# Optimization experiments

Measured on AMD Instinct MI355X. Metric: run time of the kernel, lower is better.

Reference implementation:

```python
import jax, jax.numpy as jnp
import numpy as np

B, S, D, H = 2, 2048, 1024, 16
HD = D // H          # head dim = 64
BASE = 10000.0
SCALE = 1.0 / np.sqrt(HD)


def setup_inputs() -> dict:
    key = jax.random.key(0)
    ks = jax.random.split(key, 7)
    mk = lambda k, shp: (jax.random.normal(k, shp, dtype=jnp.float32) * 0.02)
    return {
        "hidden_states": jax.random.normal(ks[0], (B, S, D), dtype=jnp.float32),
        "Wq": mk(ks[1], (D, D)), "bq": jnp.zeros((D,), jnp.float32),
        "Wk": mk(ks[2], (D, D)), "bk": jnp.zeros((D,), jnp.float32),
        "Wv": mk(ks[3], (D, D)), "bv": jnp.zeros((D,), jnp.float32),
    }


def _rope_tables(seq_len, head_dim, dtype):
    # Intended RoPE: inv_freq over head_dim/2 frequencies.
    # (Original torch code has an off-by-2 indexing bug that makes it un-runnable
    #  for head_dim > 2; we implement the intended standard RoPE:
    #  inv_freq = base^{-arange(0, head_dim, 2)/head_dim}, length head_dim//2.)
    dim_half = head_dim // 2
    inv_freq = 1.0 / (BASE ** (jnp.arange(dim_half, dtype=dtype) / dim_half))
    ang = jnp.arange(seq_len, dtype=dtype)[:, None] * inv_freq[None, :]  # [S, dim_half]
    return jnp.sin(ang), jnp.cos(ang)


def _apply_rope(x, sin, cos):
    # x: [B, H, S, HD]; sin/cos: [S, HD//2]
    dim_half = x.shape[-1] // 2
    x1, x2 = x[..., :dim_half], x[..., dim_half:]
    sin = sin[None, None]  # [1,1,S,dim_half]
    cos = cos[None, None]
    return jnp.concatenate([x1 * cos - x2 * sin, x1 * sin + x2 * cos], axis=-1)


def reference(hidden_states, Wq, bq, Wk, bk, Wv, bv):
    b, s, d = hidden_states.shape
    # QKV projections (nn.Linear: x @ W.T + b), then split heads -> [B,H,S,HD]
    def proj(W, bias):
        y = jnp.einsum("bsd,ed->bse", hidden_states, W) + bias
        return y.reshape(b, s, H, HD).transpose(0, 2, 1, 3)

    q, k, v = proj(Wq, bq), proj(Wk, bk), proj(Wv, bv)

    sin, cos = _rope_tables(s, HD, hidden_states.dtype)
    q = _apply_rope(q, sin, cos)
    k = _apply_rope(k, sin, cos)

    # Non-causal SDPA, scale = 1/sqrt(head_dim), no mask, eval mode (no dropout)
    scores = jnp.einsum("bhqd,bhkd->bhqk", q, k) * SCALE
    probs = jax.nn.softmax(scores, axis=-1)
    ctx = jnp.einsum("bhqk,bhkd->bhqd", probs, v)

    # [B,H,S,HD] -> [B,S,D]
    return ctx.transpose(0, 2, 1, 3).reshape(b, s, d)
```

## Files before the change

kernel.cpp:

```cpp
#include <hip/hip_runtime.h>
#include <hip/hip_bf16.h>
#include <math.h>

#define B_  2
#define S_  2048
#define D_  1024
#define H_  16
#define HD_ 64
#define M_  (B_*S_)
#define N3  (3*D_)
#define K_  D_
#define LOG2E 1.44269504088896340736f

typedef unsigned short u16;
typedef __bf16 bf16x8 __attribute__((ext_vector_type(8)));
typedef float  f32x4  __attribute__((ext_vector_type(4)));
typedef float  f32x16 __attribute__((ext_vector_type(16)));
typedef unsigned short u16x4 __attribute__((ext_vector_type(4)));
typedef unsigned short u16x8 __attribute__((ext_vector_type(8)));
typedef unsigned int   u32x4v __attribute__((ext_vector_type(4)));

typedef const __attribute__((address_space(1))) unsigned int gu32;
typedef __attribute__((address_space(3)))       unsigned int lu32;

__device__ __forceinline__ void gload_lds16(const void* g, void* l) {
  __builtin_amdgcn_global_load_lds((gu32*)g, (lu32*)l, 16, 0, 0);
}

__device__ __forceinline__ u16 f2bf(float f) {
  unsigned u = __builtin_bit_cast(unsigned, f);
  u += 0x7fffu + ((u >> 16) & 1u);
  return (u16)(u >> 16);
}

__device__ __forceinline__ unsigned pk2(float lo, float hi) {
  unsigned d;
  asm("v_cvt_pk_bf16_f32 %0, %1, %2" : "=v"(d) : "v"(lo), "v"(hi));
  return d;
}

__global__ void k_prep(const float* __restrict__ hs, const float* __restrict__ Wq,
                       const float* __restrict__ Wk, const float* __restrict__ Wv,
                       u16* __restrict__ Xb, u16* __restrict__ Wb) {
  const int NX = M_*D_/4, NW = D_*D_/4;
  int i = blockIdx.x * blockDim.x + threadIdx.x;
  const float4* src; u16* dst; int off;
  if (i < NX)            { src = (const float4*)hs; dst = Xb;           off = i; }
  else if (i < NX+NW)    { src = (const float4*)Wq; dst = Wb;           off = i-NX; }
  else if (i < NX+2*NW)  { src = (const float4*)Wk; dst = Wb + D_*D_;   off = i-NX-NW; }
  else                   { src = (const float4*)Wv; dst = Wb + 2*D_*D_; off = i-NX-2*NW; }
  float4 v = src[off];
  ushort4 o; o.x = f2bf(v.x); o.y = f2bf(v.y); o.z = f2bf(v.z); o.w = f2bf(v.w);
  reinterpret_cast<ushort4*>(dst)[off] = o;
}

__global__ void k_tables(float* __restrict__ sinT, float* __restrict__ cosT) {
  int gid = blockIdx.x * blockDim.x + threadIdx.x;
  int s = gid >> 5, j = gid & 31;
  float invf = (float)exp(-(double)j * (log(10000.0) / 32.0));
  float angf = (float)s * invf;
  double ang = (double)angf;
  sinT[gid] = (float)sin(ang);
  cosT[gid] = (float)cos(ang);
}

#define BM 128
#define BN 128
#define BK 64

__global__ __launch_bounds__(256) void k_gemm(const u16* __restrict__ A,
                                              const u16* __restrict__ Bm,
                                              const float* __restrict__ bq,
                                              const float* __restrict__ bk,
                                              const float* __restrict__ bv,
                                              const float* __restrict__ sinT,
                                              const float* __restrict__ cosT,
                                              u16* __restrict__ Qo,
                                              u16* __restrict__ Ko,
                                              u16* __restrict__ Vo) {
  __shared__ alignas(16) u16 As[BM*BK];
  __shared__ alignas(16) u16 Bs[BN*BK];
  const int t = threadIdx.x;
  const int l = t & 63, w = t >> 6;
  const int wr = w >> 1, wc = w & 1;
  const int lr = l & 15, lg = l >> 4;

  const int lin = blockIdx.y * (N3/BN) + blockIdx.x;
  const int wk  = (lin & 7) * 96 + (lin >> 3);
  const int m0 = (wk / (N3/BN)) * BM, n0 = (wk % (N3/BN)) * BN;

  f32x4 acc[4][4] = {};

  for (int k0 = 0; k0 < K_; k0 += BK) {
#pragma unroll
    for (int i = 0; i < 4; ++i) {
      int chunk = i*256 + t;
      int row = chunk >> 3, kc = chunk & 7;
      gload_lds16(A + (size_t)(m0+row)*K_ + k0 + kc*8, &As[chunk*8]);
    }
#pragma unroll
    for (int i = 0; i < 4; ++i) {
      int chunk = i*256 + t;
      int row = chunk >> 3, kc = chunk & 7;
      gload_lds16(Bm + (size_t)(n0+row)*K_ + k0 + kc*8, &Bs[chunk*8]);
    }
    __syncthreads();
#pragma unroll
    for (int ks = 0; ks < 2; ++ks) {
      bf16x8 a[4], b[4];
#pragma unroll
      for (int m = 0; m < 4; ++m)
        a[m] = *reinterpret_cast<const bf16x8*>(&As[(wr*64 + m*16 + lr)*BK + ks*32 + lg*8]);
#pragma unroll
      for (int n = 0; n < 4; ++n)
        b[n] = *reinterpret_cast<const bf16x8*>(&Bs[(wc*64 + n*16 + lr)*BK + ks*32 + lg*8]);
#pragma unroll
      for (int m = 0; m < 4; ++m)
#pragma unroll
        for (int n = 0; n < 4; ++n)
          acc[m][n] = __builtin_amdgcn_mfma_f32_16x16x32_bf16(a[m], b[n], acc[m][n], 0, 0, 0);
    }
    __syncthreads();
  }

  const int cw0  = n0 + wc*64;
  const int proj = cw0 >> 10;
  const int h    = (cw0 & (D_-1)) >> 6;
  const int b    = m0 >> 11;
  const int sb_  = (m0 & (S_-1)) + wr*64;

  if (proj < 2) {
    const float* bias = proj ? bk : bq;
    u16* dst = proj ? Ko : Qo;
    const float qs = proj ? 1.0f : 0.125f * LOG2E;
    float b1[2], b2[2];
#pragma unroll
    for (int n = 0; n < 2; ++n) {
      b1[n] = bias[h*HD_ + n*16 + lr];
      b2[n] = bias[h*HD_ + n*16 + lr + 32];
    }
#pragma unroll
    for (int m = 0; m < 4; ++m)
#pragma unroll
      for (int r = 0; r < 4; ++r) {
        int s = sb_ + m*16 + lg*4 + r;
        size_t orow = ((size_t)(b*H_ + h)*S_ + s)*HD_;
#pragma unroll
        for (int n = 0; n < 2; ++n) {
          int j = n*16 + lr;
          float x1 = acc[m][n][r]   + b1[n];
          float x2 = acc[m][n+2][r] + b2[n];
          float c  = cosT[(s<<5) + j], sn = sinT[(s<<5) + j];
          dst[orow + j]      = f2bf((x1*c - x2*sn) * qs);
          dst[orow + j + 32] = f2bf((x1*sn + x2*c) * qs);
        }
      }
  } else {
    float bb[4];
#pragma unroll
    for (int n = 0; n < 4; ++n) bb[n] = bv[h*HD_ + n*16 + lr];
#pragma unroll
    for (int m = 0; m < 4; ++m)
#pragma unroll
      for (int r = 0; r < 4; ++r) {
        int s = sb_ + m*16 + lg*4 + r;
        size_t orow = ((size_t)(b*H_ + h)*S_ + s)*HD_;
#pragma unroll
        for (int n = 0; n < 4; ++n)
          Vo[orow + n*16 + lr] = f2bf(acc[m][n][r] + bb[n]);
      }
  }
}

__global__ __launch_bounds__(256) void k_vt2(const u16* __restrict__ Vb,
                                             u16* __restrict__ Vt) {
  __shared__ u16 tile[64*68];
  const int bh = blockIdx.y, s0 = blockIdx.x * 64, t = threadIdx.x;
#pragma unroll
  for (int i = 0; i < 2; ++i) {
    int chunk = i*256 + t;
    int sl = chunk >> 3, c8 = chunk & 7;
    u16x8 v = *reinterpret_cast<const u16x8*>(Vb + ((size_t)bh*S_ + s0 + sl)*HD_ + c8*8);
    u16x4 lo = __builtin_shufflevector(v, v, 0, 1, 2, 3);
    u16x4 hi = __builtin_shufflevector(v, v, 4, 5, 6, 7);
    *reinterpret_cast<u16x4*>(&tile[sl*68 + c8*8])     = lo;
    *reinterpret_cast<u16x4*>(&tile[sl*68 + c8*8 + 4]) = hi;
  }
  __syncthreads();
#pragma unroll
  for (int i = 0; i < 2; ++i) {
    int chunk = i*256 + t;
    int hd = chunk >> 3, sb = chunk & 7;
    u16x8 o;
#pragma unroll
    for (int k = 0; k < 8; ++k) {
      int p   = sb*8 + k;
      int key = (p & ~15) | (p & 3) | ((p & 4) << 1) | ((p & 8) >> 1);
      o[k] = tile[key*68 + hd];
    }
    *reinterpret_cast<u16x8*>(Vt + ((size_t)bh*HD_ + hd)*S_ + s0 + sb*8) = o;
  }
}

#define QBW 32
#define NWV 4
#define QTT (QBW*NWV)
#define KTL 128
#define NTL (S_/KTL)

__global__ __launch_bounds__(256) void k_attn(const u16* __restrict__ Q,
                                              const u16* __restrict__ K,
                                              const u16* __restrict__ Vt,
                                              float* __restrict__ out) {
  __shared__ alignas(16) u16 Ks[2][KTL*HD_];
  __shared__ alignas(16) u16 Vs[2][HD_*KTL];
  __shared__ float lsums[NWV][QBW];
  const int t = threadIdx.x, l = t & 63, w = t >> 6;
  const int q32 = l & 31, hi = l >> 5;

  const int bid = blockIdx.x;
  const int work = (bid & 7) * 64 + (bid >> 3);
  const int bh = work >> 4;
  const int q0 = (work & 15) * QTT;

  const u16* Qg = Q  + ((size_t)bh*S_ + q0 + w*QBW)*HD_;
  const u16* Kg = K  + (size_t)bh*S_*HD_;
  const u16* Vg = Vt + (size_t)bh*HD_*S_;

  bf16x8 qf[4];
#pragma unroll
  for (int kt = 0; kt < 4; ++kt)
    qf[kt] = *reinterpret_cast<const bf16x8*>(Qg + (size_t)q32*HD_ + kt*16 + hi*8);

  f32x16 O0 = {}, O1 = {};
  float lsum = 0.f;

  const u16* ksrc[4]; const u16* vsrc[4];
#pragma unroll
  for (int i = 0; i < 4; ++i) {
    int g  = t + 256*i;
    int kr = g >> 3,  kc = (g & 7)  ^ (kr & 7);
    ksrc[i] = Kg + (size_t)kr*HD_ + kc*8;
    int vr = g >> 4,  vc = (g & 15) ^ (vr & 15);
    vsrc[i] = Vg + (size_t)vr*S_ + vc*8;
  }

#pragma unroll
  for (int i = 0; i < 4; ++i) {
    gload_lds16(ksrc[i], &Ks[0][(t + 256*i)*8]);
    gload_lds16(vsrc[i], &Vs[0][(t + 256*i)*8]);
  }
  __syncthreads();

  int cur = 0;
  for (int tile = 0; tile < NTL; ++tile) {
    if (tile + 1 < NTL) {
#pragma unroll
      for (int i = 0; i < 4; ++i) {
        gload_lds16(ksrc[i] + (size_t)(tile+1)*KTL*HD_, &Ks[cur^1][(t + 256*i)*8]);
        gload_lds16(vsrc[i] + (tile+1)*KTL,             &Vs[cur^1][(t + 256*i)*8]);
      }
    }

#pragma unroll
    for (int half = 0; half < 2; ++half) {
      f32x16 d0 = {}, d1 = {};
      __builtin_amdgcn_s_setprio(1);
#pragma unroll
      for (int kt = 0; kt < 4; ++kt) {
        const int gsw = ((kt*2 + hi) ^ (q32 & 7)) * 8;
        bf16x8 k0 = *reinterpret_cast<const bf16x8*>(&Ks[cur][(half*64 + q32)*HD_ + gsw]);
        d0 = __builtin_amdgcn_mfma_f32_32x32x16_bf16(k0, qf[kt], d0, 0, 0, 0);
        bf16x8 k1 = *reinterpret_cast<const bf16x8*>(&Ks[cur][(half*64 + 32 + q32)*HD_ + gsw]);
        d1 = __builtin_amdgcn_mfma_f32_32x32x16_bf16(k1, qf[kt], d1, 0, 0, 0);
      }
      __builtin_amdgcn_s_setprio(0);

      unsigned pw[4][4];
#pragma unroll
      for (int c = 0; c < 4; ++c) {
        float e[8];
#pragma unroll
        for (int i = 0; i < 8; ++i) {
          float sv = (c < 2) ? d0[(c & 1)*8 + i] : d1[(c & 1)*8 + i];
          e[i] = exp2f(sv);
          lsum += e[i];
        }
#pragma unroll
        for (int j = 0; j < 4; ++j) pw[c][j] = pk2(e[2*j], e[2*j+1]);
      }

      __builtin_amdgcn_s_setprio(1);
#pragma unroll
      for (int c = 0; c < 4; ++c) {
        u32x4v pv_ = {pw[c][0], pw[c][1], pw[c][2], pw[c][3]};
        bf16x8 pa = __builtin_bit_cast(bf16x8, pv_);
        const int gv = ((half*8 + c*2 + hi) ^ (q32 & 15)) * 8;
        bf16x8 v0 = *reinterpret_cast<const bf16x8*>(&Vs[cur][q32*KTL + gv]);
        O0 = __builtin_amdgcn_mfma_f32_32x32x16_bf16(pa, v0, O0, 0, 0, 0);
        bf16x8 v1 = *reinterpret_cast<const bf16x8*>(&Vs[cur][(32 + q32)*KTL + gv]);
        O1 = __builtin_amdgcn_mfma_f32_32x32x16_bf16(pa, v1, O1, 0, 0, 0);
      }
      __builtin_amdgcn_s_setprio(0);
    }

    __syncthreads();
    cur ^= 1;
  }

  lsum += __shfl_xor(lsum, 32);
  if (l < 32) lsums[w][l] = lsum;

  const int b = bh >> 4, h = bh & 15;
#pragma unroll
  for (int r = 0; r < 16; ++r) {
    int qrow = (r & 3) + 8*(r >> 2) + 4*hi;
    float inv = 1.f / lsums[w][qrow];
    size_t o = (size_t)(b*S_ + q0 + w*QBW + qrow)*D_ + h*HD_;
    out[o + q32]      = O0[r] * inv;
    out[o + 32 + q32] = O1[r] * inv;
  }
}

extern "C" void kernel_launch(void* const* d_in, const int* in_sizes, int n_in,
                              void* d_out, int out_size, void* d_ws, size_t ws_size,
                              hipStream_t stream) {
  const float* hs = (const float*)d_in[0];
  const float* Wq = (const float*)d_in[1];
  const float* bq = (const float*)d_in[2];
  const float* Wk = (const float*)d_in[3];
  const float* bk = (const float*)d_in[4];
  const float* Wv = (const float*)d_in[5];
  const float* bv = (const float*)d_in[6];
  float* out = (float*)d_out;

  char* ws = (char*)d_ws;
  u16*   Xb   = (u16*)  (ws);
  u16*   Wb   = (u16*)  (ws + 8388608);
  u16*   Qb   = (u16*)  (ws + 14680064);
  u16*   Kb   = (u16*)  (ws + 23068672);
  u16*   Vb   = (u16*)  (ws + 31457280);
  u16*   Vtb  = (u16*)  (ws + 39845888);
  float* sinT = (float*)(ws + 48234496);
  float* cosT = (float*)(ws + 48496640);

  k_prep<<<(M_*D_/4 + 3*(D_*D_/4)) / 256, 256, 0, stream>>>(hs, Wq, Wk, Wv, Xb, Wb);
  k_tables<<<256, 256, 0, stream>>>(sinT, cosT);
  k_gemm<<<dim3(N3/BN, M_/BM), 256, 0, stream>>>(Xb, Wb, bq, bk, bv, sinT, cosT, Qb, Kb, Vb);
  k_vt2<<<dim3(S_/64, B_*H_), 256, 0, stream>>>(Vb, Vtb);
  k_attn<<<512, 256, 0, stream>>>(Qb, Kb, Vtb, out);
}
```

Baseline: 205.8 us.

## Fuse V transpose into GEMM epilogue and merge table kernel into prep

The GEMM epilogue now writes V directly in the transposed, key-permuted layout that attention expects, so the separate transpose kernel and its round trip of V through memory go away. The sin/cos table generation is folded into the conversion kernel as extra blocks, which removes one launch. In attention, exp2f becomes the hardware exp2 builtin and the row sum is split across four partial accumulators to shorten the dependency chain. The transposed stores are 8-byte chunks strided by S, which may coalesce less well than the old transpose kernel's writes.

```diff
diff --git a/kernel.cpp b/kernel.cpp
--- a/kernel.cpp
+++ b/kernel.cpp
@@ -39,29 +39,31 @@
   return d;
 }
 
+#define NPREP ((M_*D_/4 + 3*(D_*D_/4)) / 256)
 __global__ void k_prep(const float* __restrict__ hs, const float* __restrict__ Wq,
                        const float* __restrict__ Wk, const float* __restrict__ Wv,
-                       u16* __restrict__ Xb, u16* __restrict__ Wb) {
-  const int NX = M_*D_/4, NW = D_*D_/4;
+                       u16* __restrict__ Xb, u16* __restrict__ Wb,
+                       float* __restrict__ sinT, float* __restrict__ cosT) {
+  const int NX = M_*D_/4, NW = D_*D_/4, NTOT = NX + 3*NW;
   int i = blockIdx.x * blockDim.x + threadIdx.x;
-  const float4* src; u16* dst; int off;
-  if (i < NX)            { src = (const float4*)hs; dst = Xb;           off = i; }
-  else if (i < NX+NW)    { src = (const float4*)Wq; dst = Wb;           off = i-NX; }
-  else if (i < NX+2*NW)  { src = (const float4*)Wk; dst = Wb + D_*D_;   off = i-NX-NW; }
-  else                   { src = (const float4*)Wv; dst = Wb + 2*D_*D_; off = i-NX-2*NW; }
-  float4 v = src[off];
-  ushort4 o; o.x = f2bf(v.x); o.y = f2bf(v.y); o.z = f2bf(v.z); o.w = f2bf(v.w);
-  reinterpret_cast<ushort4*>(dst)[off] = o;
-}
-
-__global__ void k_tables(float* __restrict__ sinT, float* __restrict__ cosT) {
-  int gid = blockIdx.x * blockDim.x + threadIdx.x;
-  int s = gid >> 5, j = gid & 31;
-  float invf = (float)exp(-(double)j * (log(10000.0) / 32.0));
-  float angf = (float)s * invf;
-  double ang = (double)angf;
-  sinT[gid] = (float)sin(ang);
-  cosT[gid] = (float)cos(ang);
+  if (i < NTOT) {
+    const float4* src; u16* dst; int off;
+    if (i < NX)            { src = (const float4*)hs; dst = Xb;           off = i; }
+    else if (i < NX+NW)    { src = (const float4*)Wq; dst = Wb;           off = i-NX; }
+    else if (i < NX+2*NW)  { src = (const float4*)Wk; dst = Wb + D_*D_;   off = i-NX-NW; }
+    else                   { src = (const float4*)Wv; dst = Wb + 2*D_*D_; off = i-NX-2*NW; }
+    float4 v = src[off];
+    ushort4 o; o.x = f2bf(v.x); o.y = f2bf(v.y); o.z = f2bf(v.z); o.w = f2bf(v.w);
+    reinterpret_cast<ushort4*>(dst)[off] = o;
+  } else {
+    int gid = i - NTOT;
+    int s = gid >> 5, j = gid & 31;
+    float invf = (float)exp(-(double)j * (log(10000.0) / 32.0));
+    float angf = (float)s * invf;
+    double ang = (double)angf;
+    sinT[gid] = (float)sin(ang);
+    cosT[gid] = (float)cos(ang);
+  }
 }
 
 #define BM 128
@@ -77,7 +79,7 @@
                                               const float* __restrict__ cosT,
                                               u16* __restrict__ Qo,
                                               u16* __restrict__ Ko,
-                                              u16* __restrict__ Vo) {
+                                              u16* __restrict__ Vt) {
   __shared__ alignas(16) u16 As[BM*BK];
   __shared__ alignas(16) u16 Bs[BN*BK];
   const int t = threadIdx.x;
@@ -159,46 +161,18 @@
     float bb[4];
 #pragma unroll
     for (int n = 0; n < 4; ++n) bb[n] = bv[h*HD_ + n*16 + lr];
+    const int lgp = ((lg & 1) << 1) | (lg >> 1);
+    const int pos0 = sb_ + lgp*4;
 #pragma unroll
     for (int m = 0; m < 4; ++m)
 #pragma unroll
-      for (int r = 0; r < 4; ++r) {
-        int s = sb_ + m*16 + lg*4 + r;
-        size_t orow = ((size_t)(b*H_ + h)*S_ + s)*HD_;
-#pragma unroll
-        for (int n = 0; n < 4; ++n)
-          Vo[orow + n*16 + lr] = f2bf(acc[m][n][r] + bb[n]);
-      }
-  }
-}
-
-__global__ __launch_bounds__(256) void k_vt2(const u16* __restrict__ Vb,
-                                             u16* __restrict__ Vt) {
-  __shared__ u16 tile[64*68];
-  const int bh = blockIdx.y, s0 = blockIdx.x * 64, t = threadIdx.x;
-#pragma unroll
-  for (int i = 0; i < 2; ++i) {
-    int chunk = i*256 + t;
-    int sl = chunk >> 3, c8 = chunk & 7;
-    u16x8 v = *reinterpret_cast<const u16x8*>(Vb + ((size_t)bh*S_ + s0 + sl)*HD_ + c8*8);
-    u16x4 lo = __builtin_shufflevector(v, v, 0, 1, 2, 3);
-    u16x4 hi = __builtin_shufflevector(v, v, 4, 5, 6, 7);
-    *reinterpret_cast<u16x4*>(&tile[sl*68 + c8*8])     = lo;
-    *reinterpret_cast<u16x4*>(&tile[sl*68 + c8*8 + 4]) = hi;
-  }
-  __syncthreads();
-#pragma unroll
-  for (int i = 0; i < 2; ++i) {
-    int chunk = i*256 + t;
-    int hd = chunk >> 3, sb = chunk & 7;
-    u16x8 o;
-#pragma unroll
-    for (int k = 0; k < 8; ++k) {
-      int p   = sb*8 + k;
-      int key = (p & ~15) | (p & 3) | ((p & 4) << 1) | ((p & 8) >> 1);
-      o[k] = tile[key*68 + hd];
-    }
-    *reinterpret_cast<u16x8*>(Vt + ((size_t)bh*HD_ + hd)*S_ + s0 + sb*8) = o;
+      for (int n = 0; n < 4; ++n) {
+        int hd = n*16 + lr;
+        u16x4 o;
+#pragma unroll
+        for (int r = 0; r < 4; ++r) o[r] = f2bf(acc[m][n][r] + bb[n]);
+        *reinterpret_cast<u16x4*>(Vt + ((size_t)(b*H_ + h)*HD_ + hd)*S_ + pos0 + m*16) = o;
+      }
   }
 }
 
@@ -233,7 +207,7 @@
     qf[kt] = *reinterpret_cast<const bf16x8*>(Qg + (size_t)q32*HD_ + kt*16 + hi*8);
 
   f32x16 O0 = {}, O1 = {};
-  float lsum = 0.f;
+  float lp0 = 0.f, lp1 = 0.f, lp2 = 0.f, lp3 = 0.f;
 
   const u16* ksrc[4]; const u16* vsrc[4];
 #pragma unroll
@@ -283,9 +257,12 @@
 #pragma unroll
         for (int i = 0; i < 8; ++i) {
           float sv = (c < 2) ? d0[(c & 1)*8 + i] : d1[(c & 1)*8 + i];
-          e[i] = exp2f(sv);
-          lsum += e[i];
+          e[i] = __builtin_amdgcn_exp2f(sv);
         }
+        lp0 += e[0] + e[4];
+        lp1 += e[1] + e[5];
+        lp2 += e[2] + e[6];
+        lp3 += e[3] + e[7];
 #pragma unroll
         for (int j = 0; j < 4; ++j) pw[c][j] = pk2(e[2*j], e[2*j+1]);
       }
@@ -308,6 +285,7 @@
     cur ^= 1;
   }
 
+  float lsum = (lp0 + lp1) + (lp2 + lp3);
   lsum += __shfl_xor(lsum, 32);
   if (l < 32) lsums[w][l] = lsum;
 
@@ -339,14 +317,11 @@
   u16*   Wb   = (u16*)  (ws + 8388608);
   u16*   Qb   = (u16*)  (ws + 14680064);
   u16*   Kb   = (u16*)  (ws + 23068672);
-  u16*   Vb   = (u16*)  (ws + 31457280);
-  u16*   Vtb  = (u16*)  (ws + 39845888);
-  float* sinT = (float*)(ws + 48234496);
-  float* cosT = (float*)(ws + 48496640);
-
-  k_prep<<<(M_*D_/4 + 3*(D_*D_/4)) / 256, 256, 0, stream>>>(hs, Wq, Wk, Wv, Xb, Wb);
-  k_tables<<<256, 256, 0, stream>>>(sinT, cosT);
-  k_gemm<<<dim3(N3/BN, M_/BM), 256, 0, stream>>>(Xb, Wb, bq, bk, bv, sinT, cosT, Qb, Kb, Vb);
-  k_vt2<<<dim3(S_/64, B_*H_), 256, 0, stream>>>(Vb, Vtb);
+  u16*   Vtb  = (u16*)  (ws + 31457280);
+  float* sinT = (float*)(ws + 39845888);
+  float* cosT = (float*)(ws + 40108032);
+
+  k_prep<<<NPREP + 256, 256, 0, stream>>>(hs, Wq, Wk, Wv, Xb, Wb, sinT, cosT);
+  k_gemm<<<dim3(N3/BN, M_/BM), 256, 0, stream>>>(Xb, Wb, bq, bk, bv, sinT, cosT, Qb, Kb, Vtb);
   k_attn<<<512, 256, 0, stream>>>(Qb, Kb, Vtb, out);
 }
```

Measured after the change: 183.9 us. 10.7% less time.
